# Kernel tuning notes

Hardware: AMD Instinct MI355X
Metric: run time of the kernel (lower is better)

## Reference

```python
import jax, jax.numpy as jnp
import numpy as np

B, S, D = 4, 1024, 64
NEG = -1e9


def setup_inputs() -> dict:
    key = jax.random.key(0)
    ks = jax.random.split(key, 5)
    x = jax.random.normal(ks[0], (B, S, D), dtype=jnp.float32)
    # nn.Linear weights are [out_features, in_features]
    Wq = jax.random.normal(ks[1], (D, D), dtype=jnp.float32) / np.sqrt(D)
    Wk = jax.random.normal(ks[2], (D, D), dtype=jnp.float32) / np.sqrt(D)
    bk = jax.random.normal(ks[3], (D,), dtype=jnp.float32) / np.sqrt(D)
    Wv = jax.random.normal(ks[4], (D, D), dtype=jnp.float32) / np.sqrt(D)
    attn_w = jnp.ones((3,), dtype=jnp.float32)
    attn_scale = jnp.ones((1,), dtype=jnp.float32)
    return {"x": x, "Wq": Wq, "Wk": Wk, "bk": bk, "Wv": Wv,
            "attn_w": attn_w, "attn_scale": attn_scale}


def reference(x, Wq, Wk, bk, Wv, attn_w, attn_scale):
    b, s, d = x.shape
    tril = jnp.tril(jnp.ones((s, s), dtype=bool))  # causal mask, shared by all branches

    # --- branch 1: plain causal self-attention on raw x ---
    s1 = jnp.einsum('bqd,bkd->bqk', x, x)
    s1 = jnp.where(tril, s1, NEG)
    o1 = jnp.einsum('bqk,bkd->bqd', jax.nn.softmax(s1, axis=-1), x)

    # --- branch 2: scaled dot-product attention with learned extra scale ---
    q = x @ Wq.T
    k = x @ Wk.T + bk
    v = x @ Wv.T
    inv_sqrt_d = 1.0 / float(np.sqrt(d))
    s2 = jnp.einsum('bqd,bkd->bqk', q, k) * inv_sqrt_d * attn_scale[0]
    s2 = jnp.where(tril, s2, NEG)
    o2 = jnp.einsum('bqk,bkd->bqd', jax.nn.softmax(s2, axis=-1), v)

    # --- branch 3: additive (Bahdanau-style) attention ---
    # materializes [B,S,S,D] via broadcast, as in the original
    s3 = jnp.sum(jnp.tanh(x[:, :, None, :] + x[:, None, :, :]), axis=-1)
    s3 = jnp.where(tril, s3, NEG)
    o3 = jnp.einsum('bqk,bkd->bqd', jax.nn.softmax(s3, axis=-1), x)

    w = attn_w / attn_w.sum()
    return o1 * w[0] + o2 * w[1] + o3 * w[2]


if __name__ == "__main__":
    out = reference(**setup_inputs())
    print(out.shape, out.dtype)
```

## Files before the change

### kernel.cpp

```cpp
#include <hip/hip_runtime.h>
#include <hip/hip_bf16.h>

#define BB 4
#define SS 1024
#define NSD (BB*SS*64)

typedef __attribute__((ext_vector_type(4))) float f32x4;
typedef __attribute__((ext_vector_type(8))) short bf16x8;

__device__ __forceinline__ float fast_exp2(float x) { return __builtin_amdgcn_exp2f(x); }
__device__ __forceinline__ float fast_rcp(float x)  { return __builtin_amdgcn_rcpf(x); }

__device__ __forceinline__ unsigned short f2bf(float f) {
    unsigned int u = __builtin_bit_cast(unsigned int, f);
    u += 0x7fffu + ((u >> 16) & 1u);
    return (unsigned short)(u >> 16);
}
__device__ __forceinline__ float bf2f(unsigned short u) {
    unsigned int v = (unsigned int)u << 16;
    return __builtin_bit_cast(float, v);
}

__device__ __forceinline__ float sig4(const f32x4 eq, const f32x4 ek) {
    float A = __builtin_fmaf(eq[0], ek[0], 1.0f);
    float B = __builtin_fmaf(eq[1], ek[1], 1.0f);
    float C = __builtin_fmaf(eq[2], ek[2], 1.0f);
    float D = __builtin_fmaf(eq[3], ek[3], 1.0f);
    float AB = A*B, CD = C*D;
    float num = __builtin_fmaf(A+B, CD, (C+D)*AB);
    return num * fast_rcp(AB*CD);
}

__global__ __launch_bounds__(256) void k_proj(
    const float* __restrict__ x, const float* __restrict__ Wq,
    const float* __restrict__ Wk, const float* __restrict__ bkv,
    const float* __restrict__ Wv,
    unsigned short* __restrict__ qh, unsigned short* __restrict__ ql,
    unsigned short* __restrict__ kh, unsigned short* __restrict__ kl,
    unsigned short* __restrict__ xh, unsigned short* __restrict__ xlo,
    float* __restrict__ exf,
    unsigned short* __restrict__ xT, unsigned short* __restrict__ vT)
{
    __shared__ float xsh[4*68];
    const int t = threadIdx.x;
    const int r = t & 3, cc = t >> 2;
    const int row0 = blockIdx.x * 4;
    if (t < 64) {
        const int rr = t >> 4, seg = (t & 15) * 4;
        *(f32x4*)(xsh + rr*68 + seg) =
            *(const f32x4*)(x + (size_t)(row0 + rr)*64 + seg);
    }
    __syncthreads();

    const float* wqp = Wq + cc*64;
    const float* wkp = Wk + cc*64;
    const float* wvp = Wv + cc*64;
    float aq = 0.f, ak = 0.f, av = 0.f;
    #pragma unroll 4
    for (int e0 = 0; e0 < 64; e0 += 4) {
        f32x4 xv = *(const f32x4*)(xsh + r*68 + e0);
        f32x4 q4 = *(const f32x4*)(wqp + e0);
        f32x4 k4 = *(const f32x4*)(wkp + e0);
        f32x4 v4 = *(const f32x4*)(wvp + e0);
        #pragma unroll
        for (int u = 0; u < 4; ++u) {
            aq = __builtin_fmaf(xv[u], q4[u], aq);
            ak = __builtin_fmaf(xv[u], k4[u], ak);
            av = __builtin_fmaf(xv[u], v4[u], av);
        }
    }
    const int row = row0 + r;
    const int b = row >> 10, srow = row & 1023;
    const float C2 = 2.8853900817779268f;
    ak += bkv[cc];
    const size_t idx = (size_t)row*64 + cc;
    unsigned short h;
    h = f2bf(aq); qh[idx] = h; ql[idx] = f2bf(aq - bf2f(h));
    h = f2bf(ak); kh[idx] = h; kl[idx] = f2bf(ak - bf2f(h));
    const float xv_ = xsh[r*68 + cc];
    h = f2bf(xv_); xh[idx] = h; xlo[idx] = f2bf(xv_ - bf2f(h));
    exf[idx] = fast_exp2(C2 * xv_);
    xT[((size_t)b*64 + cc)*1024 + srow] = h;
    vT[((size_t)b*64 + cc)*1024 + srow] = f2bf(av);
}

__global__ __launch_bounds__(256) void k_fused(
    const unsigned short* __restrict__ xh, const unsigned short* __restrict__ xlo,
    const unsigned short* __restrict__ qh, const unsigned short* __restrict__ ql,
    const unsigned short* __restrict__ kh, const unsigned short* __restrict__ kl,
    const float* __restrict__ exf,
    const unsigned short* __restrict__ xT, const unsigned short* __restrict__ vT,
    const float* __restrict__ attn_scale,
    float* __restrict__ po, float* __restrict__ lb)
{
    __shared__ float sexq[32*68];
    __shared__ float sexk[64*68];
    __shared__ unsigned short Pl[32*72];
    __shared__ float lpart[4][16];
    __shared__ float l_arr[32];

    const int t = threadIdx.x;
    const int bx = blockIdx.x;
    const int lane = t & 63, wv = t >> 6;
    const int l15 = lane & 15, g = lane >> 4;
    const float LOG2E = 1.4426950408889634f;

    if (bx < 512) {
        const int s4 = bx & 3, b = (bx >> 2) & 3;
        const int qt3 = 31 - (bx >> 4);
        const int q0 = qt3 * 32;
        const int nc = (qt3 >> 1) + 1;

        {
            const int rw = t >> 3, seg = (t & 7) * 8;
            const float* gsrc = exf + ((size_t)b*SS + q0 + rw)*64 + seg;
            f32x4* dst = (f32x4*)(sexq + rw*68 + seg);
            dst[0] = ((const f32x4*)gsrc)[0];
            dst[1] = ((const f32x4*)gsrc)[1];
        }
        __syncthreads();

        const int qp = t >> 4, kb = t & 15;
        const int qh_w = wv & 1, dbase = (wv >> 1) * 32;
        float lacc0 = 0.f, lacc1 = 0.f;
        f32x4 oacc0 = {0,0,0,0}, oacc1 = {0,0,0,0};

        for (int c = s4; c < nc; c += 4) {
            const int kc = c * 64;
            {
                const int rw = t >> 2, seg = (t & 3) * 16;
                const float* gsrc = exf + ((size_t)b*SS + kc + rw)*64 + seg;
                f32x4* dst = (f32x4*)(sexk + rw*68 + seg);
                #pragma unroll
                for (int i = 0; i < 4; ++i) dst[i] = ((const f32x4*)gsrc)[i];
            }
            __syncthreads();

            float ar0[4] = {0.f,0.f,0.f,0.f};
            float ar1[4] = {0.f,0.f,0.f,0.f};
            #pragma unroll 4
            for (int d0 = 0; d0 < 64; d0 += 4) {
                f32x4 eq0 = *(const f32x4*)(sexq + (qp*2+0)*68 + d0);
                f32x4 eq1 = *(const f32x4*)(sexq + (qp*2+1)*68 + d0);
                #pragma unroll
                for (int j = 0; j < 4; ++j) {
                    f32x4 ek = *(const f32x4*)(sexk + (kb + 16*j)*68 + d0);
                    ar0[j] += sig4(eq0, ek);
                    ar1[j] += sig4(eq1, ek);
                }
            }
            #pragma unroll
            for (int j = 0; j < 4; ++j) {
                const int kg = kc + kb + 16*j;
                float e0 = (kg <= q0 + qp*2 + 0)
                    ? fast_exp2(__builtin_fmaf(ar0[j], -2.8853900817779268f, 46.166241308446475f)) : 0.f;
                float e1 = (kg <= q0 + qp*2 + 1)
                    ? fast_exp2(__builtin_fmaf(ar1[j], -2.8853900817779268f, 46.166241308446475f)) : 0.f;
                lacc0 += e0; lacc1 += e1;
                Pl[(qp*2+0)*72 + kb + 16*j] = f2bf(e0);
                Pl[(qp*2+1)*72 + kb + 16*j] = f2bf(e1);
            }
            __syncthreads();
            const unsigned short* vb = xT + (size_t)b*64*1024;
            #pragma unroll
            for (int ks = 0; ks < 2; ++ks) {
                bf16x8 af = *(const bf16x8*)(Pl + (qh_w*16 + l15)*72 + ks*32 + g*8);
                bf16x8 b0 = *(const bf16x8*)(vb + (size_t)(dbase + l15)*1024 + kc + ks*32 + g*8);
                bf16x8 b1 = *(const bf16x8*)(vb + (size_t)(dbase + 16 + l15)*1024 + kc + ks*32 + g*8);
                oacc0 = __builtin_amdgcn_mfma_f32_16x16x32_bf16(af, b0, oacc0, 0, 0, 0);
                oacc1 = __builtin_amdgcn_mfma_f32_16x16x32_bf16(af, b1, oacc1, 0, 0, 0);
            }
            __syncthreads();
        }
        #pragma unroll
        for (int off = 8; off >= 1; off >>= 1) {
            lacc0 += __shfl_xor(lacc0, off, 64);
            lacc1 += __shfl_xor(lacc1, off, 64);
        }
        if (kb == 0) { l_arr[qp*2] = lacc0; l_arr[qp*2+1] = lacc1; }
        __syncthreads();
        const size_t slot = 4 + s4;
        if (t < 32) lb[slot*((size_t)BB*SS) + (size_t)b*SS + q0 + t] = l_arr[t];
        float* pob = po + slot*((size_t)NSD) + ((size_t)b*SS + q0)*64;
        #pragma unroll
        for (int i = 0; i < 4; ++i) {
            const int rr = qh_w*16 + g*4 + i;
            pob[(size_t)rr*64 + dbase + l15]      = oacc0[i];
            pob[(size_t)rr*64 + dbase + 16 + l15] = oacc1[i];
        }
    } else {
        const int y = bx - 512;
        const int split = y & 1, b = (y >> 1) & 3;
        const int qt = 63 - ((y >> 3) & 63);
        const int br = (y >> 9) & 1;
        const int q0 = qt * 16;
        const int nc = (qt >> 2) + 1;

        const unsigned short* Ah_p = (br ? qh : xh) + ((size_t)b*SS + q0)*64;
        const unsigned short* Al_p = (br ? ql : xlo) + ((size_t)b*SS + q0)*64;
        const unsigned short* Bh_p = (br ? kh : xh) + (size_t)b*SS*64;
        const unsigned short* Bl_p = (br ? kl : xlo) + (size_t)b*SS*64;
        const unsigned short* Vb   = (br ? vT : xT) + (size_t)b*64*1024;

        const int ko = g * 8;
        bf16x8 Ah0 = *(const bf16x8*)(Ah_p + (size_t)l15*64 + ko);
        bf16x8 Ah1 = *(const bf16x8*)(Ah_p + (size_t)l15*64 + 32 + ko);
        bf16x8 Al0 = *(const bf16x8*)(Al_p + (size_t)l15*64 + ko);
        bf16x8 Al1 = *(const bf16x8*)(Al_p + (size_t)l15*64 + 32 + ko);

        const float pscale = br ? (0.125f * attn_scale[0] * LOG2E) : LOG2E;
        const float pshift = br ? 0.f : (-64.f * LOG2E);

        f32x4 lacc = {0,0,0,0};
        f32x4 oacc = {0,0,0,0};

        for (int c = split; c < nc; c += 2) {
            const int kc = c * 64;
            const int krow = kc + wv*16 + l15;
            bf16x8 Bh0 = *(const bf16x8*)(Bh_p + (size_t)krow*64 + ko);
            bf16x8 Bh1 = *(const bf16x8*)(Bh_p + (size_t)krow*64 + 32 + ko);
            bf16x8 Bl0 = *(const bf16x8*)(Bl_p + (size_t)krow*64 + ko);
            bf16x8 Bl1 = *(const bf16x8*)(Bl_p + (size_t)krow*64 + 32 + ko);
            f32x4 s = {0,0,0,0};
            s = __builtin_amdgcn_mfma_f32_16x16x32_bf16(Ah0, Bh0, s, 0, 0, 0);
            s = __builtin_amdgcn_mfma_f32_16x16x32_bf16(Ah1, Bh1, s, 0, 0, 0);
            s = __builtin_amdgcn_mfma_f32_16x16x32_bf16(Ah0, Bl0, s, 0, 0, 0);
            s = __builtin_amdgcn_mfma_f32_16x16x32_bf16(Ah1, Bl1, s, 0, 0, 0);
            s = __builtin_amdgcn_mfma_f32_16x16x32_bf16(Al0, Bh0, s, 0, 0, 0);
            s = __builtin_amdgcn_mfma_f32_16x16x32_bf16(Al1, Bh1, s, 0, 0, 0);
            const int kg = kc + wv*16 + l15;
            #pragma unroll
            for (int i = 0; i < 4; ++i) {
                const int q = q0 + g*4 + i;
                float e = (kg <= q) ? fast_exp2(__builtin_fmaf(s[i], pscale, pshift)) : 0.f;
                lacc[i] += e;
                Pl[(g*4+i)*72 + wv*16 + l15] = f2bf(e);
            }
            __syncthreads();
            #pragma unroll
            for (int ks = 0; ks < 2; ++ks) {
                bf16x8 af = *(const bf16x8*)(Pl + l15*72 + ks*32 + g*8);
                bf16x8 bf_ = *(const bf16x8*)(Vb + (size_t)(wv*16 + l15)*1024 + kc + ks*32 + g*8);
                oacc = __builtin_amdgcn_mfma_f32_16x16x32_bf16(af, bf_, oacc, 0, 0, 0);
            }
            __syncthreads();
        }
        #pragma unroll
        for (int off = 8; off >= 1; off >>= 1) {
            lacc[0] += __shfl_xor(lacc[0], off, 64);
            lacc[1] += __shfl_xor(lacc[1], off, 64);
            lacc[2] += __shfl_xor(lacc[2], off, 64);
            lacc[3] += __shfl_xor(lacc[3], off, 64);
        }
        if (l15 == 0) {
            #pragma unroll
            for (int i = 0; i < 4; ++i) lpart[wv][g*4 + i] = lacc[i];
        }
        __syncthreads();
        const size_t slot = (size_t)(br*2 + split);
        if (t < 16) {
            float l = lpart[0][t] + lpart[1][t] + lpart[2][t] + lpart[3][t];
            lb[slot*((size_t)BB*SS) + (size_t)b*SS + q0 + t] = l;
        }
        float* pob = po + slot*((size_t)NSD) + ((size_t)b*SS + q0)*64;
        #pragma unroll
        for (int i = 0; i < 4; ++i)
            pob[(size_t)(g*4 + i)*64 + wv*16 + l15] = oacc[i];
    }
}

__global__ __launch_bounds__(256) void k_comb(
    const float* __restrict__ po, const float* __restrict__ lb,
    const float* __restrict__ attn_w, float* __restrict__ out)
{
    const int v = blockIdx.x*256 + threadIdx.x;
    const int qg = v >> 4;
    const float aw0 = attn_w[0], aw1 = attn_w[1], aw2 = attn_w[2];
    const float iws = fast_rcp(aw0 + aw1 + aw2);
    const f32x4* p = (const f32x4*)po;
    const int NQ = BB*SS;

    f32x4 s01 = p[(size_t)0*65536 + v] + p[(size_t)1*65536 + v];
    f32x4 s23 = p[(size_t)2*65536 + v] + p[(size_t)3*65536 + v];
    f32x4 s47 = (p[(size_t)4*65536 + v] + p[(size_t)5*65536 + v])
              + (p[(size_t)6*65536 + v] + p[(size_t)7*65536 + v]);
    const float f0 = aw0 * iws * fast_rcp(lb[0*NQ + qg] + lb[1*NQ + qg]);
    const float f1 = aw1 * iws * fast_rcp(lb[2*NQ + qg] + lb[3*NQ + qg]);
    const float f2 = aw2 * iws * fast_rcp(lb[4*NQ + qg] + lb[5*NQ + qg]
                                        + lb[6*NQ + qg] + lb[7*NQ + qg]);
    f32x4 o;
    #pragma unroll
    for (int u = 0; u < 4; ++u)
        o[u] = __builtin_fmaf(s01[u], f0,
               __builtin_fmaf(s23[u], f1, s47[u]*f2));
    ((f32x4*)out)[v] = o;
}

extern "C" void kernel_launch(void* const* d_in, const int* in_sizes, int n_in,
                              void* d_out, int out_size, void* d_ws, size_t ws_size,
                              hipStream_t stream) {
    (void)in_sizes; (void)n_in; (void)out_size; (void)ws_size;
    const float* x          = (const float*)d_in[0];
    const float* Wq         = (const float*)d_in[1];
    const float* Wk         = (const float*)d_in[2];
    const float* bk         = (const float*)d_in[3];
    const float* Wv         = (const float*)d_in[4];
    const float* attn_w     = (const float*)d_in[5];
    const float* attn_scale = (const float*)d_in[6];
    float* out              = (float*)d_out;

    float* exf = (float*)d_ws;
    unsigned short* qh  = (unsigned short*)(exf + NSD);
    unsigned short* ql  = qh  + NSD;
    unsigned short* kh  = ql  + NSD;
    unsigned short* kl  = kh  + NSD;
    unsigned short* xh  = kl  + NSD;
    unsigned short* xlo = xh  + NSD;
    unsigned short* xT  = xlo + NSD;
    unsigned short* vT  = xT  + NSD;
    float* po = (float*)(vT + NSD);
    float* lb = po + (size_t)8*NSD;

    k_proj <<<1024, 256, 0, stream>>>(x, Wq, Wk, bk, Wv,
                                      qh, ql, kh, kl, xh, xlo, exf, xT, vT);
    k_fused<<<1536, 256, 0, stream>>>(xh, xlo, qh, ql, kh, kl, exf, xT, vT,
                                      attn_scale, po, lb);
    k_comb <<<256, 256, 0, stream>>>(po, lb, attn_w, out);
}
```

Measured before the change: 50.57 us.

## Restructure additive-attention branch to per-wave tiles with 8-way key split

The additive-attention path drops the block-level LDS staging and barriers. Each wave now owns a 16-query tile, builds the probability fragment directly in registers and feeds it straight into MFMA. Key work is split 8 ways instead of 4, and the combine kernel sums 8 partial slots for that branch. The aim is to remove sync and LDS overhead and improve load balance. The cost is that the exp-feature rows are reloaded from global memory or cache per wave with no shared reuse, and the workspace partial-output traffic grows.

Measured after the change: 66.88 us. 32.3% more time.

```diff
diff --git a/kernel.cpp b/kernel.cpp
--- a/kernel.cpp
+++ b/kernel.cpp
@@ -93,11 +93,8 @@
     const float* __restrict__ attn_scale,
     float* __restrict__ po, float* __restrict__ lb)
 {
-    __shared__ float sexq[32*68];
-    __shared__ float sexk[64*68];
-    __shared__ unsigned short Pl[32*72];
+    __shared__ unsigned short Pl[16*72];
     __shared__ float lpart[4][16];
-    __shared__ float l_arr[32];
 
     const int t = threadIdx.x;
     const int bx = blockIdx.x;
@@ -106,87 +103,68 @@
     const float LOG2E = 1.4426950408889634f;
 
     if (bx < 512) {
-        const int s4 = bx & 3, b = (bx >> 2) & 3;
-        const int qt3 = 31 - (bx >> 4);
-        const int q0 = qt3 * 32;
-        const int nc = (qt3 >> 1) + 1;
-
-        {
-            const int rw = t >> 3, seg = (t & 7) * 8;
-            const float* gsrc = exf + ((size_t)b*SS + q0 + rw)*64 + seg;
-            f32x4* dst = (f32x4*)(sexq + rw*68 + seg);
-            dst[0] = ((const f32x4*)gsrc)[0];
-            dst[1] = ((const f32x4*)gsrc)[1];
-        }
-        __syncthreads();
-
-        const int qp = t >> 4, kb = t & 15;
-        const int qh_w = wv & 1, dbase = (wv >> 1) * 32;
-        float lacc0 = 0.f, lacc1 = 0.f;
-        f32x4 oacc0 = {0,0,0,0}, oacc1 = {0,0,0,0};
-
-        for (int c = s4; c < nc; c += 4) {
-            const int kc = c * 64;
-            {
-                const int rw = t >> 2, seg = (t & 3) * 16;
-                const float* gsrc = exf + ((size_t)b*SS + kc + rw)*64 + seg;
-                f32x4* dst = (f32x4*)(sexk + rw*68 + seg);
-                #pragma unroll
-                for (int i = 0; i < 4; ++i) dst[i] = ((const f32x4*)gsrc)[i];
-            }
-            __syncthreads();
-
-            float ar0[4] = {0.f,0.f,0.f,0.f};
-            float ar1[4] = {0.f,0.f,0.f,0.f};
+        const int w = bx*4 + wv;
+        const int s8 = w & 7, b = (w >> 3) & 3;
+        const int qt = 63 - (w >> 5);
+        const int q0 = qt * 16;
+        const int q = q0 + l15;
+        const int nsteps = (qt >> 1) + 1;
+
+        const float* eqp = exf + ((size_t)b*SS + q0 + l15)*64;
+        const float* ekb = exf + (size_t)b*SS*64;
+        const unsigned short* vb = xT + (size_t)b*64*1024;
+
+        f32x4 a0 = {0,0,0,0}, a1 = {0,0,0,0}, a2 = {0,0,0,0}, a3 = {0,0,0,0};
+        float lsum = 0.f;
+
+        for (int c = s8; c < nsteps; c += 8) {
+            const int kc = c * 32;
+            const int kb0 = kc + g*8;
+            const float* ekp = ekb + (size_t)kb0*64;
+            float ar[8] = {0.f,0.f,0.f,0.f,0.f,0.f,0.f,0.f};
             #pragma unroll 4
             for (int d0 = 0; d0 < 64; d0 += 4) {
-                f32x4 eq0 = *(const f32x4*)(sexq + (qp*2+0)*68 + d0);
-                f32x4 eq1 = *(const f32x4*)(sexq + (qp*2+1)*68 + d0);
+                f32x4 eqv = *(const f32x4*)(eqp + d0);
                 #pragma unroll
-                for (int j = 0; j < 4; ++j) {
-                    f32x4 ek = *(const f32x4*)(sexk + (kb + 16*j)*68 + d0);
-                    ar0[j] += sig4(eq0, ek);
-                    ar1[j] += sig4(eq1, ek);
+                for (int jj = 0; jj < 8; ++jj) {
+                    f32x4 ekv = *(const f32x4*)(ekp + (size_t)jj*64 + d0);
+                    ar[jj] += sig4(eqv, ekv);
                 }
             }
+            bf16x8 af;
             #pragma unroll
-            for (int j = 0; j < 4; ++j) {
-                const int kg = kc + kb + 16*j;
-                float e0 = (kg <= q0 + qp*2 + 0)
-                    ? fast_exp2(__builtin_fmaf(ar0[j], -2.8853900817779268f, 46.166241308446475f)) : 0.f;
-                float e1 = (kg <= q0 + qp*2 + 1)
-                    ? fast_exp2(__builtin_fmaf(ar1[j], -2.8853900817779268f, 46.166241308446475f)) : 0.f;
-                lacc0 += e0; lacc1 += e1;
-                Pl[(qp*2+0)*72 + kb + 16*j] = f2bf(e0);
-                Pl[(qp*2+1)*72 + kb + 16*j] = f2bf(e1);
+            for (int jj = 0; jj < 8; ++jj) {
+                float e = (kb0 + jj <= q)
+                    ? fast_exp2(__builtin_fmaf(ar[jj], -2.8853900817779268f,
+                                               46.166241308446475f))
+                    : 0.f;
+                lsum += e;
+                af[jj] = (short)f2bf(e);
             }
-            __syncthreads();
-            const unsigned short* vb = xT + (size_t)b*64*1024;
-            #pragma unroll
-            for (int ks = 0; ks < 2; ++ks) {
-                bf16x8 af = *(const bf16x8*)(Pl + (qh_w*16 + l15)*72 + ks*32 + g*8);
-                bf16x8 b0 = *(const bf16x8*)(vb + (size_t)(dbase + l15)*1024 + kc + ks*32 + g*8);
-                bf16x8 b1 = *(const bf16x8*)(vb + (size_t)(dbase + 16 + l15)*1024 + kc + ks*32 + g*8);
-                oacc0 = __builtin_amdgcn_mfma_f32_16x16x32_bf16(af, b0, oacc0, 0, 0, 0);
-                oacc1 = __builtin_amdgcn_mfma_f32_16x16x32_bf16(af, b1, oacc1, 0, 0, 0);
-            }
-            __syncthreads();
-        }
-        #pragma unroll
-        for (int off = 8; off >= 1; off >>= 1) {
-            lacc0 += __shfl_xor(lacc0, off, 64);
-            lacc1 += __shfl_xor(lacc1, off, 64);
-        }
-        if (kb == 0) { l_arr[qp*2] = lacc0; l_arr[qp*2+1] = lacc1; }
-        __syncthreads();
-        const size_t slot = 4 + s4;
-        if (t < 32) lb[slot*((size_t)BB*SS) + (size_t)b*SS + q0 + t] = l_arr[t];
-        float* pob = po + slot*((size_t)NSD) + ((size_t)b*SS + q0)*64;
+            bf16x8 b0 = *(const bf16x8*)(vb + (size_t)( 0 + l15)*1024 + kb0);
+            bf16x8 b1 = *(const bf16x8*)(vb + (size_t)(16 + l15)*1024 + kb0);
+            bf16x8 b2 = *(const bf16x8*)(vb + (size_t)(32 + l15)*1024 + kb0);
+            bf16x8 b3 = *(const bf16x8*)(vb + (size_t)(48 + l15)*1024 + kb0);
+            a0 = __builtin_amdgcn_mfma_f32_16x16x32_bf16(af, b0, a0, 0, 0, 0);
+            a1 = __builtin_amdgcn_mfma_f32_16x16x32_bf16(af, b1, a1, 0, 0, 0);
+            a2 = __builtin_amdgcn_mfma_f32_16x16x32_bf16(af, b2, a2, 0, 0, 0);
+            a3 = __builtin_amdgcn_mfma_f32_16x16x32_bf16(af, b3, a3, 0, 0, 0);
+        }
+
+        lsum += __shfl_xor(lsum, 16, 64);
+        lsum += __shfl_xor(lsum, 32, 64);
+
+        const size_t slot = 4 + s8;
+        if (lane < 16)
+            lb[slot*(size_t)(BB*SS) + (size_t)b*SS + q0 + lane] = lsum;
+        float* pob = po + slot*(size_t)NSD + ((size_t)b*SS + q0)*64;
         #pragma unroll
         for (int i = 0; i < 4; ++i) {
-            const int rr = qh_w*16 + g*4 + i;
-            pob[(size_t)rr*64 + dbase + l15]      = oacc0[i];
-            pob[(size_t)rr*64 + dbase + 16 + l15] = oacc1[i];
+            const int rr = g*4 + i;
+            pob[(size_t)rr*64 +  0 + l15] = a0[i];
+            pob[(size_t)rr*64 + 16 + l15] = a1[i];
+            pob[(size_t)rr*64 + 32 + l15] = a2[i];
+            pob[(size_t)rr*64 + 48 + l15] = a3[i];
         }
     } else {
         const int y = bx - 512;
@@ -282,17 +260,21 @@
 
     f32x4 s01 = p[(size_t)0*65536 + v] + p[(size_t)1*65536 + v];
     f32x4 s23 = p[(size_t)2*65536 + v] + p[(size_t)3*65536 + v];
-    f32x4 s47 = (p[(size_t)4*65536 + v] + p[(size_t)5*65536 + v])
-              + (p[(size_t)6*65536 + v] + p[(size_t)7*65536 + v]);
+    f32x4 s3s = {0,0,0,0};
+    float l3 = 0.f;
+    #pragma unroll
+    for (int s = 4; s < 12; ++s) {
+        s3s += p[(size_t)s*65536 + v];
+        l3 += lb[s*NQ + qg];
+    }
     const float f0 = aw0 * iws * fast_rcp(lb[0*NQ + qg] + lb[1*NQ + qg]);
     const float f1 = aw1 * iws * fast_rcp(lb[2*NQ + qg] + lb[3*NQ + qg]);
-    const float f2 = aw2 * iws * fast_rcp(lb[4*NQ + qg] + lb[5*NQ + qg]
-                                        + lb[6*NQ + qg] + lb[7*NQ + qg]);
+    const float f2 = aw2 * iws * fast_rcp(l3);
     f32x4 o;
     #pragma unroll
     for (int u = 0; u < 4; ++u)
         o[u] = __builtin_fmaf(s01[u], f0,
-               __builtin_fmaf(s23[u], f1, s47[u]*f2));
+               __builtin_fmaf(s23[u], f1, s3s[u]*f2));
     ((f32x4*)out)[v] = o;
 }
 
@@ -319,7 +301,7 @@
     unsigned short* xT  = xlo + NSD;
     unsigned short* vT  = xT  + NSD;
     float* po = (float*)(vT + NSD);
-    float* lb = po + (size_t)8*NSD;
+    float* lb = po + (size_t)12*NSD;
 
     k_proj <<<1024, 256, 0, stream>>>(x, Wq, Wk, bk, Wv,
                                       qh, ql, kh, kl, xh, xlo, exf, xT, vT);
```
